# Optimization experiments

Measured on AMD Instinct MI355X. Metric: run time of the kernel, lower is better.

The kernel has to match this reference:

```python
import jax, jax.numpy as jnp
import numpy as np

HIDDEN_DIM = 64  # self.hidden_dim = inc
N = 16384
C = 64


def setup_inputs() -> dict:
    key = jax.random.key(0)
    k1, k2, k3, k4, k5 = jax.random.split(key, 5)
    scale = 1.0 / np.sqrt(C)
    return {
        "hidden": jax.random.normal(k1, (N, C), dtype=jnp.float32),
        "query": jax.random.normal(k2, (N, C), dtype=jnp.float32),
        "Wq": jax.random.normal(k3, (C, C), dtype=jnp.float32) * scale,
        "Wk": jax.random.normal(k4, (C, C), dtype=jnp.float32) * scale,
        "Wv": jax.random.normal(k5, (C, C), dtype=jnp.float32) * scale,
    }


def reference(hidden, query, Wq, Wk, Wv):
    # Per-voxel linear projections (center-tap of the sparse 3x3x3 convs)
    q = query @ Wq            # [Nq, C]
    k = hidden @ Wk           # [Nk, C]
    v = hidden @ Wv           # [Nk, C]
    # score = q @ k.T / sqrt(hidden_dim)
    score = jnp.einsum("qc,kc->qk", q, k) / jnp.sqrt(jnp.float32(HIDDEN_DIM))
    attn = jax.nn.softmax(score, axis=-1)  # [Nq, Nk]
    weight = attn @ v         # [Nq, C] -> new hidden.F
    return weight
```

## Files before the change

### kernel.cpp

```cpp
#include <hip/hip_runtime.h>
#include <hip/hip_bf16.h>

#define NT 16384
#define CD 64

typedef __attribute__((ext_vector_type(8))) short bf16x8;
typedef __attribute__((ext_vector_type(16))) float f32x16;
typedef __attribute__((ext_vector_type(2))) int int2v;

#define AS1 __attribute__((address_space(1)))
#define AS3 __attribute__((address_space(3)))

__global__ __launch_bounds__(256) void proj_kernel(
    const float* __restrict__ hidden, const float* __restrict__ query,
    const float* __restrict__ Wq, const float* __restrict__ Wk, const float* __restrict__ Wv,
    __hip_bfloat16* __restrict__ qb, __hip_bfloat16* __restrict__ kb,
    __hip_bfloat16* __restrict__ vTb)
{
    __shared__ float qin[32][64];
    __shared__ float hin[32][64];
    const int tid = threadIdx.x;
    const int R0 = blockIdx.x * 32;
    {
        int r = tid >> 3, c0 = (tid & 7) * 8;
        const float4* qs = (const float4*)(query + (size_t)(R0 + r) * CD + c0);
        const float4* hs = (const float4*)(hidden + (size_t)(R0 + r) * CD + c0);
        *(float4*)&qin[r][c0]     = qs[0];
        *(float4*)&qin[r][c0 + 4] = qs[1];
        *(float4*)&hin[r][c0]     = hs[0];
        *(float4*)&hin[r][c0 + 4] = hs[1];
    }
    __syncthreads();
    const int c = tid & 63, rg = tid >> 6;
    const float SC = 0.18033688011112042f;
    float aq[8] = {0.f}, ak[8] = {0.f}, av[8] = {0.f};
    #pragma unroll 4
    for (int j = 0; j < 64; ++j) {
        float wq = Wq[j * 64 + c], wk = Wk[j * 64 + c], wv = Wv[j * 64 + c];
        #pragma unroll
        for (int r8 = 0; r8 < 8; ++r8) {
            float qv = qin[rg * 8 + r8][j];
            float hv = hin[rg * 8 + r8][j];
            aq[r8] += qv * wq;
            ak[r8] += hv * wk;
            av[r8] += hv * wv;
        }
    }
    #pragma unroll
    for (int r8 = 0; r8 < 8; ++r8) {
        int row = R0 + rg * 8 + r8;
        qb[(size_t)row * CD + c] = __float2bfloat16(aq[r8] * SC);
        kb[(size_t)row * CD + c] = __float2bfloat16(ak[r8]);
    }
    union { bf16x8 v; __hip_bfloat16 h[8]; } u;
    #pragma unroll
    for (int r8 = 0; r8 < 8; ++r8) u.h[r8] = __float2bfloat16(av[r8]);
    *(bf16x8*)(vTb + (size_t)c * NT + R0 + rg * 8) = u.v;
}

__device__ __forceinline__ void stage_tiles(
    char* kdst, char* vdst,
    const __hip_bfloat16* kb, const __hip_bfloat16* vTb,
    int kv, int wid, int lane)
{
    const char* kt = (const char*)(kb + (size_t)kv * CD);
    #pragma unroll
    for (int j = 0; j < 2; ++j) {
        int ob = (wid * 2 + j) * 1024;
        int o  = ob + lane * 16;
        int so = o ^ (((o >> 7) & 7) << 4);
        __builtin_amdgcn_global_load_lds((const AS1 void*)(kt + so),
                                         (AS3 void*)(kdst + ob), 16, 0, 0);
    }
    #pragma unroll
    for (int j = 0; j < 2; ++j) {
        int ob = (wid * 2 + j) * 1024;
        int o  = ob + lane * 16;
        int c  = o >> 7;
        int colb = (o & 127) ^ ((c & 7) << 4);
        __builtin_amdgcn_global_load_lds(
            (const AS1 void*)((const char*)vTb + ((size_t)c * NT + kv) * 2 + colb),
            (AS3 void*)(vdst + ob), 16, 0, 0);
    }
}

__device__ __forceinline__ void softpack_half(
    const f32x16& s, float& lsum, int paw[2][4])
{
    float p[16];
    #pragma unroll
    for (int r = 0; r < 16; ++r) p[r] = __builtin_amdgcn_exp2f(s[r]);
    {
        float t0 = ((p[0] + p[1]) + (p[2] + p[3])) + ((p[4] + p[5]) + (p[6] + p[7]));
        float t1 = ((p[8] + p[9]) + (p[10] + p[11])) + ((p[12] + p[13]) + (p[14] + p[15]));
        lsum += t0 + t1;
    }
    int w[8];
    #pragma unroll
    for (int r2 = 0; r2 < 4; ++r2)
        #pragma unroll
        for (int u = 0; u < 2; ++u)
            asm("v_cvt_pk_bf16_f32 %0, %1, %2"
                : "=v"(w[r2 * 2 + u]) : "v"(p[4*r2 + 2*u]), "v"(p[4*r2 + 2*u + 1]));
    #pragma unroll
    for (int r2e = 0; r2e < 4; r2e += 2)
        #pragma unroll
        for (int u = 0; u < 2; ++u) {
            int2v ra = __builtin_amdgcn_permlane32_swap(w[r2e*2 + u], w[(r2e+1)*2 + u], false, false);
            paw[r2e >> 1][u]     = ra.x;
            paw[r2e >> 1][2 + u] = ra.y;
        }
}

__global__ __launch_bounds__(256, 3) void flash_kernel(
    const __hip_bfloat16* __restrict__ qb, const __hip_bfloat16* __restrict__ kb,
    const __hip_bfloat16* __restrict__ vTb,
    __hip_bfloat16* __restrict__ part, float* __restrict__ lbuf, float* __restrict__ out,
    int nsplit, int kvlen)
{
    __shared__ __align__(16) char kbuf[2][8192];
    __shared__ __align__(16) char vbuf[2][8192];
    __shared__ float llds[4][64];

    const int tid  = threadIdx.x;
    const int lane = tid & 63, wid = tid >> 6;
    const int l31 = lane & 31, h = lane >> 5;
    const int split = blockIdx.x % nsplit;
    const int qblk  = blockIdx.x / nsplit;
    const int q0  = qblk * 256 + wid * 64;
    const int kv0 = split * kvlen;
    const int ntile = kvlen / 64;

    bf16x8 QfA[4], QfB[4];
    #pragma unroll
    for (int cc = 0; cc < 4; ++cc) {
        QfA[cc] = *(const bf16x8*)(qb + (size_t)(q0 + l31) * CD + cc * 16 + h * 8);
        QfB[cc] = *(const bf16x8*)(qb + (size_t)(q0 + 32 + l31) * CD + cc * 16 + h * 8);
    }

    f32x16 accA[2], accB[2];
    #pragma unroll
    for (int dt = 0; dt < 2; ++dt) {
        #pragma unroll
        for (int r = 0; r < 16; ++r) { accA[dt][r] = 0.f; accB[dt][r] = 0.f; }
    }
    float lsumA = 0.f, lsumB = 0.f;

    const int krow0 = l31, krow1 = 32 + l31;
    const int kswz  = (l31 & 7) << 4;

    stage_tiles(kbuf[0], vbuf[0], kb, vTb, kv0, wid, lane);
    asm volatile("s_waitcnt vmcnt(0)" ::: "memory");
    __syncthreads();

    for (int t = 0; t < ntile; ++t) {
        const int b = t & 1;
        if (t + 1 < ntile)
            stage_tiles(kbuf[b ^ 1], vbuf[b ^ 1], kb, vTb, kv0 + (t + 1) * 64, wid, lane);

        #pragma unroll
        for (int half = 0; half < 2; ++half) {
            const int krow = half ? krow1 : krow0;
            f32x16 sA, sB;
            #pragma unroll
            for (int r = 0; r < 16; ++r) { sA[r] = 0.f; sB[r] = 0.f; }
            __builtin_amdgcn_s_setprio(1);
            #pragma unroll
            for (int cc = 0; cc < 4; ++cc) {
                bf16x8 k0 = *(const bf16x8*)(kbuf[b] + krow * 128 + ((cc * 32 + h * 16) ^ kswz));
                sA = __builtin_amdgcn_mfma_f32_32x32x16_bf16(k0, QfA[cc], sA, 0, 0, 0);
                sB = __builtin_amdgcn_mfma_f32_32x32x16_bf16(k0, QfB[cc], sB, 0, 0, 0);
            }
            __builtin_amdgcn_s_setprio(0);

            int pA[2][4], pB[2][4];
            softpack_half(sA, lsumA, pA);
            softpack_half(sB, lsumB, pB);

            __builtin_amdgcn_s_setprio(1);
            #pragma unroll
            for (int j = 0; j < 2; ++j) {
                const int colb = ((half * 2 + j) * 32 + h * 16) ^ kswz;
                bf16x8 v0 = *(const bf16x8*)(vbuf[b] + krow0 * 128 + colb);
                bf16x8 v1 = *(const bf16x8*)(vbuf[b] + krow1 * 128 + colb);
                union { int i[4]; bf16x8 v; } puA, puB;
                #pragma unroll
                for (int jj = 0; jj < 4; ++jj) { puA.i[jj] = pA[j][jj]; puB.i[jj] = pB[j][jj]; }
                accA[0] = __builtin_amdgcn_mfma_f32_32x32x16_bf16(puA.v, v0, accA[0], 0, 0, 0);
                accA[1] = __builtin_amdgcn_mfma_f32_32x32x16_bf16(puA.v, v1, accA[1], 0, 0, 0);
                accB[0] = __builtin_amdgcn_mfma_f32_32x32x16_bf16(puB.v, v0, accB[0], 0, 0, 0);
                accB[1] = __builtin_amdgcn_mfma_f32_32x32x16_bf16(puB.v, v1, accB[1], 0, 0, 0);
            }
            __builtin_amdgcn_s_setprio(0);
        }

        asm volatile("s_waitcnt vmcnt(0)" ::: "memory");
        __syncthreads();
    }

    float lfA = lsumA + __shfl_xor(lsumA, 32);
    float lfB = lsumB + __shfl_xor(lsumB, 32);

    if (nsplit == 1) {
        llds[wid][l31] = lfA;
        llds[wid][32 + l31] = lfB;
        __builtin_amdgcn_wave_barrier();
        #pragma unroll
        for (int dt = 0; dt < 2; ++dt)
            #pragma unroll
            for (int r = 0; r < 16; ++r) {
                int qrow = (r & 3) + 8 * (r >> 2) + 4 * h;
                out[(size_t)(q0 + qrow) * CD + dt * 32 + l31]      = accA[dt][r] / llds[wid][qrow];
                out[(size_t)(q0 + 32 + qrow) * CD + dt * 32 + l31] = accB[dt][r] / llds[wid][32 + qrow];
            }
    } else {
        __hip_bfloat16* pb = part + ((size_t)split * NT + q0) * CD;
        #pragma unroll
        for (int dt = 0; dt < 2; ++dt)
            #pragma unroll
            for (int r = 0; r < 16; ++r) {
                int qrow = (r & 3) + 8 * (r >> 2) + 4 * h;
                pb[qrow * CD + dt * 32 + l31]        = __float2bfloat16(accA[dt][r]);
                pb[(32 + qrow) * CD + dt * 32 + l31] = __float2bfloat16(accB[dt][r]);
            }
        if (h == 0) {
            lbuf[(size_t)split * NT + q0 + l31]      = lfA;
            lbuf[(size_t)split * NT + q0 + 32 + l31] = lfB;
        }
    }
}

__global__ __launch_bounds__(256) void combine_kernel(
    const __hip_bfloat16* __restrict__ part, const float* __restrict__ lbuf,
    float* __restrict__ out, int S)
{
    const int tid = threadIdx.x;
    const int row = blockIdx.x * 4 + (tid >> 6);
    const int c = tid & 63;
    float L = 0.f, o = 0.f;
    for (int s = 0; s < S; ++s) {
        L += lbuf[(size_t)s * NT + row];
        o += __bfloat162float(part[((size_t)s * NT + row) * CD + c]);
    }
    out[(size_t)row * CD + c] = o / L;
}

extern "C" void kernel_launch(void* const* d_in, const int* in_sizes, int n_in,
                              void* d_out, int out_size, void* d_ws, size_t ws_size,
                              hipStream_t stream)
{
    (void)in_sizes; (void)n_in; (void)out_size;
    const float* hidden = (const float*)d_in[0];
    const float* query  = (const float*)d_in[1];
    const float* Wq = (const float*)d_in[2];
    const float* Wk = (const float*)d_in[3];
    const float* Wv = (const float*)d_in[4];
    float* out = (float*)d_out;

    char* ws = (char*)d_ws;
    __hip_bfloat16* qb  = (__hip_bfloat16*)ws;
    __hip_bfloat16* kb  = qb + (size_t)NT * CD;
    __hip_bfloat16* vTb = kb + (size_t)NT * CD;
    const size_t base = (size_t)3 * NT * CD * 2;
    const size_t per  = (size_t)NT * CD * 2 + (size_t)NT * 4;

    int S = 1;
    if (ws_size >= base + 16 * per) S = 16;
    else if (ws_size >= base + 8 * per) S = 8;
    else if (ws_size >= base + 4 * per) S = 4;
    else if (ws_size >= base + 2 * per) S = 2;

    __hip_bfloat16* part = (__hip_bfloat16*)(ws + base);
    float* lbuf = (float*)(ws + base + (size_t)S * NT * CD * 2);

    hipLaunchKernelGGL(proj_kernel, dim3(NT / 32), dim3(256), 0, stream,
                       hidden, query, Wq, Wk, Wv, qb, kb, vTb);
    hipLaunchKernelGGL(flash_kernel, dim3((NT / 256) * S), dim3(256), 0, stream,
                       qb, kb, vTb, part, lbuf, out, S, NT / S);
    if (S > 1)
        hipLaunchKernelGGL(combine_kernel, dim3(NT / 4), dim3(256), 0, stream,
                           part, lbuf, out, S);
}
```

Baseline: 111.3 us.

## Software-pipeline QK and PV across tiles with triple buffering, halve per-wave rows

Each wave now handles 32 query rows instead of 64. The block covers 128 queries, so the grid doubles. The loop is restructured so that the QK^T MFMAs for tile t overlap with the softmax and PV MFMAs of tile t-1, using a 3-deep K/V LDS ring. This aims to hide softmax latency behind matrix work and to cut register pressure. The trade-off is that each K/V tile loaded into LDS is reused by half as many queries, doubling global and LDS traffic per query, and LDS use per block grows, which may limit occupancy.

```diff
diff --git a/kernel.cpp b/kernel.cpp
--- a/kernel.cpp
+++ b/kernel.cpp
@@ -118,33 +118,30 @@
     __hip_bfloat16* __restrict__ part, float* __restrict__ lbuf, float* __restrict__ out,
     int nsplit, int kvlen)
 {
-    __shared__ __align__(16) char kbuf[2][8192];
-    __shared__ __align__(16) char vbuf[2][8192];
-    __shared__ float llds[4][64];
+    __shared__ __align__(16) char kbuf[3][8192];
+    __shared__ __align__(16) char vbuf[3][8192];
+    __shared__ float llds[4][32];
 
     const int tid  = threadIdx.x;
     const int lane = tid & 63, wid = tid >> 6;
     const int l31 = lane & 31, h = lane >> 5;
     const int split = blockIdx.x % nsplit;
     const int qblk  = blockIdx.x / nsplit;
-    const int q0  = qblk * 256 + wid * 64;
+    const int q0  = qblk * 128 + wid * 32;
     const int kv0 = split * kvlen;
     const int ntile = kvlen / 64;
 
-    bf16x8 QfA[4], QfB[4];
-    #pragma unroll
-    for (int cc = 0; cc < 4; ++cc) {
-        QfA[cc] = *(const bf16x8*)(qb + (size_t)(q0 + l31) * CD + cc * 16 + h * 8);
-        QfB[cc] = *(const bf16x8*)(qb + (size_t)(q0 + 32 + l31) * CD + cc * 16 + h * 8);
-    }
-
-    f32x16 accA[2], accB[2];
-    #pragma unroll
-    for (int dt = 0; dt < 2; ++dt) {
-        #pragma unroll
-        for (int r = 0; r < 16; ++r) { accA[dt][r] = 0.f; accB[dt][r] = 0.f; }
-    }
-    float lsumA = 0.f, lsumB = 0.f;
+    bf16x8 Qf[4];
+    #pragma unroll
+    for (int cc = 0; cc < 4; ++cc)
+        Qf[cc] = *(const bf16x8*)(qb + (size_t)(q0 + l31) * CD + cc * 16 + h * 8);
+
+    f32x16 acc[2];
+    #pragma unroll
+    for (int dt = 0; dt < 2; ++dt)
+        #pragma unroll
+        for (int r = 0; r < 16; ++r) acc[dt][r] = 0.f;
+    float lsum = 0.f;
 
     const int krow0 = l31, krow1 = 32 + l31;
     const int kswz  = (l31 & 7) << 4;
@@ -152,81 +149,116 @@
     stage_tiles(kbuf[0], vbuf[0], kb, vTb, kv0, wid, lane);
     asm volatile("s_waitcnt vmcnt(0)" ::: "memory");
     __syncthreads();
-
-    for (int t = 0; t < ntile; ++t) {
-        const int b = t & 1;
+    if (ntile > 1)
+        stage_tiles(kbuf[1], vbuf[1], kb, vTb, kv0 + 64, wid, lane);
+
+    f32x16 sP0, sP1;
+    {
+        f32x16 a0, a1;
+        #pragma unroll
+        for (int r = 0; r < 16; ++r) { a0[r] = 0.f; a1[r] = 0.f; }
+        __builtin_amdgcn_s_setprio(1);
+        #pragma unroll
+        for (int cc = 0; cc < 4; ++cc) {
+            int colb = (cc * 32 + h * 16) ^ kswz;
+            bf16x8 k0 = *(const bf16x8*)(kbuf[0] + krow0 * 128 + colb);
+            bf16x8 k1 = *(const bf16x8*)(kbuf[0] + krow1 * 128 + colb);
+            a0 = __builtin_amdgcn_mfma_f32_32x32x16_bf16(k0, Qf[cc], a0, 0, 0, 0);
+            a1 = __builtin_amdgcn_mfma_f32_32x32x16_bf16(k1, Qf[cc], a1, 0, 0, 0);
+        }
+        __builtin_amdgcn_s_setprio(0);
+        sP0 = a0; sP1 = a1;
+    }
+    asm volatile("s_waitcnt vmcnt(0)" ::: "memory");
+    __syncthreads();
+
+    int prv = 0, cur = 1;
+    for (int t = 1; t < ntile; ++t) {
+        int nxt = cur + 1; if (nxt == 3) nxt = 0;
         if (t + 1 < ntile)
-            stage_tiles(kbuf[b ^ 1], vbuf[b ^ 1], kb, vTb, kv0 + (t + 1) * 64, wid, lane);
-
-        #pragma unroll
-        for (int half = 0; half < 2; ++half) {
-            const int krow = half ? krow1 : krow0;
-            f32x16 sA, sB;
+            stage_tiles(kbuf[nxt], vbuf[nxt], kb, vTb, kv0 + (t + 1) * 64, wid, lane);
+
+        f32x16 sN0, sN1;
+        #pragma unroll
+        for (int r = 0; r < 16; ++r) { sN0[r] = 0.f; sN1[r] = 0.f; }
+        const char* kbp = kbuf[cur];
+        __builtin_amdgcn_s_setprio(1);
+        #pragma unroll
+        for (int cc = 0; cc < 4; ++cc) {
+            int colb = (cc * 32 + h * 16) ^ kswz;
+            bf16x8 k0 = *(const bf16x8*)(kbp + krow0 * 128 + colb);
+            bf16x8 k1 = *(const bf16x8*)(kbp + krow1 * 128 + colb);
+            sN0 = __builtin_amdgcn_mfma_f32_32x32x16_bf16(k0, Qf[cc], sN0, 0, 0, 0);
+            sN1 = __builtin_amdgcn_mfma_f32_32x32x16_bf16(k1, Qf[cc], sN1, 0, 0, 0);
+        }
+        __builtin_amdgcn_s_setprio(0);
+
+        int pa[2][4], pb[2][4];
+        softpack_half(sP0, lsum, pa);
+        softpack_half(sP1, lsum, pb);
+
+        const char* vbp = vbuf[prv];
+        __builtin_amdgcn_s_setprio(1);
+        #pragma unroll
+        for (int kc = 0; kc < 4; ++kc) {
+            int colb = (kc * 32 + h * 16) ^ kswz;
+            bf16x8 v0 = *(const bf16x8*)(vbp + krow0 * 128 + colb);
+            bf16x8 v1 = *(const bf16x8*)(vbp + krow1 * 128 + colb);
+            union { int i[4]; bf16x8 v; } pu;
             #pragma unroll
-            for (int r = 0; r < 16; ++r) { sA[r] = 0.f; sB[r] = 0.f; }
-            __builtin_amdgcn_s_setprio(1);
-            #pragma unroll
-            for (int cc = 0; cc < 4; ++cc) {
-                bf16x8 k0 = *(const bf16x8*)(kbuf[b] + krow * 128 + ((cc * 32 + h * 16) ^ kswz));
-                sA = __builtin_amdgcn_mfma_f32_32x32x16_bf16(k0, QfA[cc], sA, 0, 0, 0);
-                sB = __builtin_amdgcn_mfma_f32_32x32x16_bf16(k0, QfB[cc], sB, 0, 0, 0);
-            }
-            __builtin_amdgcn_s_setprio(0);
-
-            int pA[2][4], pB[2][4];
-            softpack_half(sA, lsumA, pA);
-            softpack_half(sB, lsumB, pB);
-
-            __builtin_amdgcn_s_setprio(1);
-            #pragma unroll
-            for (int j = 0; j < 2; ++j) {
-                const int colb = ((half * 2 + j) * 32 + h * 16) ^ kswz;
-                bf16x8 v0 = *(const bf16x8*)(vbuf[b] + krow0 * 128 + colb);
-                bf16x8 v1 = *(const bf16x8*)(vbuf[b] + krow1 * 128 + colb);
-                union { int i[4]; bf16x8 v; } puA, puB;
-                #pragma unroll
-                for (int jj = 0; jj < 4; ++jj) { puA.i[jj] = pA[j][jj]; puB.i[jj] = pB[j][jj]; }
-                accA[0] = __builtin_amdgcn_mfma_f32_32x32x16_bf16(puA.v, v0, accA[0], 0, 0, 0);
-                accA[1] = __builtin_amdgcn_mfma_f32_32x32x16_bf16(puA.v, v1, accA[1], 0, 0, 0);
-                accB[0] = __builtin_amdgcn_mfma_f32_32x32x16_bf16(puB.v, v0, accB[0], 0, 0, 0);
-                accB[1] = __builtin_amdgcn_mfma_f32_32x32x16_bf16(puB.v, v1, accB[1], 0, 0, 0);
-            }
-            __builtin_amdgcn_s_setprio(0);
-        }
-
+            for (int j = 0; j < 4; ++j) pu.i[j] = (kc < 2) ? pa[kc][j] : pb[kc - 2][j];
+            acc[0] = __builtin_amdgcn_mfma_f32_32x32x16_bf16(pu.v, v0, acc[0], 0, 0, 0);
+            acc[1] = __builtin_amdgcn_mfma_f32_32x32x16_bf16(pu.v, v1, acc[1], 0, 0, 0);
+        }
+        __builtin_amdgcn_s_setprio(0);
+
+        sP0 = sN0; sP1 = sN1;
         asm volatile("s_waitcnt vmcnt(0)" ::: "memory");
         __syncthreads();
-    }
-
-    float lfA = lsumA + __shfl_xor(lsumA, 32);
-    float lfB = lsumB + __shfl_xor(lsumB, 32);
+        prv = cur; cur = nxt;
+    }
+
+    {
+        int pa[2][4], pb[2][4];
+        softpack_half(sP0, lsum, pa);
+        softpack_half(sP1, lsum, pb);
+        const char* vbp = vbuf[prv];
+        #pragma unroll
+        for (int kc = 0; kc < 4; ++kc) {
+            int colb = (kc * 32 + h * 16) ^ kswz;
+            bf16x8 v0 = *(const bf16x8*)(vbp + krow0 * 128 + colb);
+            bf16x8 v1 = *(const bf16x8*)(vbp + krow1 * 128 + colb);
+            union { int i[4]; bf16x8 v; } pu;
+            #pragma unroll
+            for (int j = 0; j < 4; ++j) pu.i[j] = (kc < 2) ? pa[kc][j] : pb[kc - 2][j];
+            acc[0] = __builtin_amdgcn_mfma_f32_32x32x16_bf16(pu.v, v0, acc[0], 0, 0, 0);
+            acc[1] = __builtin_amdgcn_mfma_f32_32x32x16_bf16(pu.v, v1, acc[1], 0, 0, 0);
+        }
+    }
+
+    float lfull = lsum + __shfl_xor(lsum, 32);
 
     if (nsplit == 1) {
-        llds[wid][l31] = lfA;
-        llds[wid][32 + l31] = lfB;
+        llds[wid][l31] = lfull;
         __builtin_amdgcn_wave_barrier();
         #pragma unroll
         for (int dt = 0; dt < 2; ++dt)
             #pragma unroll
             for (int r = 0; r < 16; ++r) {
                 int qrow = (r & 3) + 8 * (r >> 2) + 4 * h;
-                out[(size_t)(q0 + qrow) * CD + dt * 32 + l31]      = accA[dt][r] / llds[wid][qrow];
-                out[(size_t)(q0 + 32 + qrow) * CD + dt * 32 + l31] = accB[dt][r] / llds[wid][32 + qrow];
+                out[(size_t)(q0 + qrow) * CD + dt * 32 + l31] = acc[dt][r] / llds[wid][qrow];
             }
     } else {
-        __hip_bfloat16* pb = part + ((size_t)split * NT + q0) * CD;
+        __hip_bfloat16* pb2 = part + ((size_t)split * NT + q0) * CD;
         #pragma unroll
         for (int dt = 0; dt < 2; ++dt)
             #pragma unroll
             for (int r = 0; r < 16; ++r) {
                 int qrow = (r & 3) + 8 * (r >> 2) + 4 * h;
-                pb[qrow * CD + dt * 32 + l31]        = __float2bfloat16(accA[dt][r]);
-                pb[(32 + qrow) * CD + dt * 32 + l31] = __float2bfloat16(accB[dt][r]);
+                pb2[qrow * CD + dt * 32 + l31] = __float2bfloat16(acc[dt][r]);
             }
-        if (h == 0) {
-            lbuf[(size_t)split * NT + q0 + l31]      = lfA;
-            lbuf[(size_t)split * NT + q0 + 32 + l31] = lfB;
-        }
+        if (h == 0)
+            lbuf[(size_t)split * NT + q0 + l31] = lfull;
     }
 }
 
@@ -275,7 +307,7 @@
 
     hipLaunchKernelGGL(proj_kernel, dim3(NT / 32), dim3(256), 0, stream,
                        hidden, query, Wq, Wk, Wv, qb, kb, vTb);
-    hipLaunchKernelGGL(flash_kernel, dim3((NT / 256) * S), dim3(256), 0, stream,
+    hipLaunchKernelGGL(flash_kernel, dim3((NT / 128) * S), dim3(256), 0, stream,
                        qb, kb, vTb, part, lbuf, out, S, NT / S);
     if (S > 1)
         hipLaunchKernelGGL(combine_kernel, dim3(NT / 4), dim3(256), 0, stream,
```

Result: no change. 112.6 us (+1.1%).
